# Kernel optimization log

Hardware: AMD Instinct MI355X
Metric: run time of the kernel (lower is better)

Reference implementation:

```python
import jax, jax.numpy as jnp
import numpy as np

SCS = 15000.0          # subcarrier_spacing_hz
FS = 30720000.0        # sampling_freq_hz
FACTOR = 1.5           # ebno_to_snr_factor
MAX_CFO = 0.05
NUM_TAPS = 5
PAD = (NUM_TAPS - 1) // 2

B, N = 64, 131072


def setup_inputs() -> dict:
    key = jax.random.key(0)
    ks = jax.random.split(key, 8)
    return {
        "x_real": jax.random.normal(ks[0], (B, N), jnp.float32),
        "x_imag": jax.random.normal(ks[1], (B, N), jnp.float32),
        "ebno_db": jax.random.uniform(ks[2], (B,), jnp.float32),
        "cfo_u": jax.random.uniform(ks[3], (B, 1), jnp.float32),
        "taps_real": jax.random.normal(ks[4], (B, NUM_TAPS), jnp.float32),
        "taps_imag": jax.random.normal(ks[5], (B, NUM_TAPS), jnp.float32),
        "noise_real": jax.random.normal(ks[6], (B, N), jnp.float32),
        "noise_imag": jax.random.normal(ks[7], (B, N), jnp.float32),
    }


def _depthwise_conv(x, taps):
    # torch F.conv1d (cross-correlation) with groups=batch, padding=PAD.
    # x: [B, N], taps: [B, K] -> y[b, n] = sum_k taps[b, k] * xpad[b, n + k]
    xp = jnp.pad(x, ((0, 0), (PAD, PAD)))
    n = x.shape[1]
    return sum(taps[:, k:k + 1] * xp[:, k:k + n] for k in range(NUM_TAPS))


def _forward(x_real, x_imag, ebno_db, cfo_u, taps_real, taps_imag,
             noise_real, noise_imag):
    # --- Residual CFO: x * exp(i * 2*pi * delta_f * t) ---
    cfo_norm = (cfo_u * 2.0 - 1.0) * MAX_CFO            # [B, 1]
    delta_f = cfo_norm * SCS
    t = jnp.arange(x_real.shape[1], dtype=jnp.float32) / FS  # [N]
    phase = 2.0 * jnp.pi * delta_f * t                  # [B, N]
    c, s = jnp.cos(phase), jnp.sin(phase)
    xr = x_real * c - x_imag * s
    xi = x_real * s + x_imag * c
    # --- TDL fading: complex depthwise conv with per-sample taps ---
    yr = _depthwise_conv(xr, taps_real) - _depthwise_conv(xi, taps_imag)
    yi = _depthwise_conv(xr, taps_imag) + _depthwise_conv(xi, taps_real)
    # --- AWGN ---
    snr_db = ebno_db + 10.0 * jnp.log10(jnp.float32(FACTOR))  # [B]
    noise_std = jnp.sqrt(10.0 ** (-snr_db / 10.0))            # [B]
    # torch.randn_like(complex) has per-component std 1/sqrt(2); scaled by std/sqrt(2)
    scale = (noise_std / 2.0)[:, None]
    yr = yr + noise_real * scale
    yi = yi + noise_imag * scale
    return jnp.stack([yr, yi], axis=0)  # [2, B, N]


def reference(x_real, x_imag, ebno_db, cfo_u, taps_real, taps_imag,
              noise_real, noise_imag):
    return _forward(x_real, x_imag, ebno_db, cfo_u, taps_real, taps_imag,
                    noise_real, noise_imag)
```

## Files before the change

kernel.cpp:

```cpp
#include <hip/hip_runtime.h>
#include <math.h>

#define BB   64
#define NN   131072
#define KTAPS 5
#define TILE 1024
#define NTHREADS 256

#define ANG_PER_HZ 2.0453077171808549e-7f
#define EBNO_OFF   1.7609125905568124f
#define L2TEN_OVER20 0.16609640474436813f

typedef float f32x4 __attribute__((ext_vector_type(4)));

__global__ __launch_bounds__(NTHREADS) void wc_kernel(
    const float* __restrict__ x_real,  const float* __restrict__ x_imag,
    const float* __restrict__ ebno_db, const float* __restrict__ cfo_u,
    const float* __restrict__ taps_real, const float* __restrict__ taps_imag,
    const float* __restrict__ noise_real, const float* __restrict__ noise_imag,
    float* __restrict__ out)
{
    const int b    = blockIdx.y;
    const int base = blockIdx.x * TILE + threadIdx.x * 4;
    const size_t rowoff = (size_t)b * NN;

    const float* __restrict__ xr = x_real + rowoff;
    const float* __restrict__ xi = x_imag + rowoff;

    const int aL = (base == 0)       ? 0        : base - 4;
    const int aR = (base == NN - 4)  ? NN - 4   : base + 4;

    const float4 xrL = *reinterpret_cast<const float4*>(xr + aL);
    const float4 xr0 = *reinterpret_cast<const float4*>(xr + base);
    const float4 xrR = *reinterpret_cast<const float4*>(xr + aR);
    const float4 xiL = *reinterpret_cast<const float4*>(xi + aL);
    const float4 xi0 = *reinterpret_cast<const float4*>(xi + base);
    const float4 xiR = *reinterpret_cast<const float4*>(xi + aR);
    const float4 nr4 = *reinterpret_cast<const float4*>(noise_real + rowoff + base);
    const float4 ni4 = *reinterpret_cast<const float4*>(noise_imag + rowoff + base);

    const float cfo     = cfo_u[b];
    const float delta_f = (cfo * 2.0f - 1.0f) * 0.05f * 15000.0f;
    const float ang     = delta_f * ANG_PER_HZ;
    const float snr     = ebno_db[b] + EBNO_OFF;
    const float scale   = 0.5f * exp2f(-snr * L2TEN_OVER20);

    float tr[KTAPS], ti[KTAPS];
#pragma unroll
    for (int k = 0; k < KTAPS; ++k) {
        tr[k] = taps_real[b * KTAPS + k];
        ti[k] = taps_imag[b * KTAPS + k];
    }

    float sA, cA, s, c;
    sincosf(ang, &sA, &cA);
    sincosf(ang * (float)(base - 2), &s, &c);

    const bool lok = (base != 0);
    const bool rok = (base != NN - 4);

    float ur[8], ui[8];
    ur[0] = lok ? xrL.z : 0.0f;  ui[0] = lok ? xiL.z : 0.0f;
    ur[1] = lok ? xrL.w : 0.0f;  ui[1] = lok ? xiL.w : 0.0f;
    ur[2] = xr0.x;  ui[2] = xi0.x;
    ur[3] = xr0.y;  ui[3] = xi0.y;
    ur[4] = xr0.z;  ui[4] = xi0.z;
    ur[5] = xr0.w;  ui[5] = xi0.w;
    ur[6] = rok ? xrR.x : 0.0f;  ui[6] = rok ? xiR.x : 0.0f;
    ur[7] = rok ? xrR.y : 0.0f;  ui[7] = rok ? xiR.y : 0.0f;

    float wr[8], wi[8];
#pragma unroll
    for (int j = 0; j < 8; ++j) {
        wr[j] = ur[j] * c - ui[j] * s;
        wi[j] = ur[j] * s + ui[j] * c;
        float cn = c * cA - s * sA;
        float sn = s * cA + c * sA;
        c = cn; s = sn;
    }

    const float nr_[4] = {nr4.x, nr4.y, nr4.z, nr4.w};
    const float ni_[4] = {ni4.x, ni4.y, ni4.z, ni4.w};

    f32x4 yr4, yi4;
#pragma unroll
    for (int j = 0; j < 4; ++j) {
        float ar = 0.0f, ai = 0.0f;
#pragma unroll
        for (int k = 0; k < KTAPS; ++k) {
            ar = fmaf(tr[k], wr[j + k], ar);
            ar = fmaf(-ti[k], wi[j + k], ar);
            ai = fmaf(ti[k], wr[j + k], ai);
            ai = fmaf(tr[k], wi[j + k], ai);
        }
        yr4[j] = fmaf(nr_[j], scale, ar);
        yi4[j] = fmaf(ni_[j], scale, ai);
    }

    __builtin_nontemporal_store(yr4, reinterpret_cast<f32x4*>(out + rowoff + base));
    __builtin_nontemporal_store(yi4, reinterpret_cast<f32x4*>(out + (size_t)BB * NN + rowoff + base));
}

extern "C" void kernel_launch(void* const* d_in, const int* in_sizes, int n_in,
                              void* d_out, int out_size, void* d_ws, size_t ws_size,
                              hipStream_t stream) {
    const float* x_real     = (const float*)d_in[0];
    const float* x_imag     = (const float*)d_in[1];
    const float* ebno_db    = (const float*)d_in[2];
    const float* cfo_u      = (const float*)d_in[3];
    const float* taps_real  = (const float*)d_in[4];
    const float* taps_imag  = (const float*)d_in[5];
    const float* noise_real = (const float*)d_in[6];
    const float* noise_imag = (const float*)d_in[7];

    dim3 grid(NN / TILE, BB);
    wc_kernel<<<grid, NTHREADS, 0, stream>>>(
        x_real, x_imag, ebno_db, cfo_u, taps_real, taps_imag,
        noise_real, noise_imag, (float*)d_out);
}
```

Baseline: 180.8 us.

## Process four tiles per block with software-pipelined prefetch and narrower halo loads

Each block now handles four consecutive 1024-element chunks, loading the next chunk's inputs before computing and storing the current one, so loads overlap compute. Halo loads shrink from float4 to float2, which cuts redundant bytes. Per-row setup (taps, sincos of the step angle, noise scale) is amortized over four chunks. The grid shrinks fourfold and register pressure rises, which may reduce occupancy on a purely bandwidth-bound kernel.

```diff
diff --git a/kernel.cpp b/kernel.cpp
--- a/kernel.cpp
+++ b/kernel.cpp
@@ -5,6 +5,8 @@
 #define NN   131072
 #define KTAPS 5
 #define TILE 1024
+#define CHUNKS 4
+#define SPAN (TILE * CHUNKS)
 #define NTHREADS 256
 
 #define ANG_PER_HZ 2.0453077171808549e-7f
@@ -13,61 +15,49 @@
 
 typedef float f32x4 __attribute__((ext_vector_type(4)));
 
-__global__ __launch_bounds__(NTHREADS) void wc_kernel(
-    const float* __restrict__ x_real,  const float* __restrict__ x_imag,
-    const float* __restrict__ ebno_db, const float* __restrict__ cfo_u,
-    const float* __restrict__ taps_real, const float* __restrict__ taps_imag,
-    const float* __restrict__ noise_real, const float* __restrict__ noise_imag,
-    float* __restrict__ out)
-{
-    const int b    = blockIdx.y;
-    const int base = blockIdx.x * TILE + threadIdx.x * 4;
-    const size_t rowoff = (size_t)b * NN;
+struct Buf {
+    float2 xrL, xrR, xiL, xiR;
+    float4 xr0, xi0, nr, ni;
+};
 
-    const float* __restrict__ xr = x_real + rowoff;
-    const float* __restrict__ xi = x_imag + rowoff;
+__device__ __forceinline__ Buf load_chunk(const float* __restrict__ xr,
+                                          const float* __restrict__ xi,
+                                          const float* __restrict__ nr,
+                                          const float* __restrict__ ni,
+                                          int base) {
+    const int aL = (base == 0)      ? 0      : base - 2;
+    const int aR = (base == NN - 4) ? NN - 2 : base + 4;
+    Buf b;
+    b.xrL = *reinterpret_cast<const float2*>(xr + aL);
+    b.xr0 = *reinterpret_cast<const float4*>(xr + base);
+    b.xrR = *reinterpret_cast<const float2*>(xr + aR);
+    b.xiL = *reinterpret_cast<const float2*>(xi + aL);
+    b.xi0 = *reinterpret_cast<const float4*>(xi + base);
+    b.xiR = *reinterpret_cast<const float2*>(xi + aR);
+    b.nr  = *reinterpret_cast<const float4*>(nr + base);
+    b.ni  = *reinterpret_cast<const float4*>(ni + base);
+    return b;
+}
 
-    const int aL = (base == 0)       ? 0        : base - 4;
-    const int aR = (base == NN - 4)  ? NN - 4   : base + 4;
-
-    const float4 xrL = *reinterpret_cast<const float4*>(xr + aL);
-    const float4 xr0 = *reinterpret_cast<const float4*>(xr + base);
-    const float4 xrR = *reinterpret_cast<const float4*>(xr + aR);
-    const float4 xiL = *reinterpret_cast<const float4*>(xi + aL);
-    const float4 xi0 = *reinterpret_cast<const float4*>(xi + base);
-    const float4 xiR = *reinterpret_cast<const float4*>(xi + aR);
-    const float4 nr4 = *reinterpret_cast<const float4*>(noise_real + rowoff + base);
-    const float4 ni4 = *reinterpret_cast<const float4*>(noise_imag + rowoff + base);
-
-    const float cfo     = cfo_u[b];
-    const float delta_f = (cfo * 2.0f - 1.0f) * 0.05f * 15000.0f;
-    const float ang     = delta_f * ANG_PER_HZ;
-    const float snr     = ebno_db[b] + EBNO_OFF;
-    const float scale   = 0.5f * exp2f(-snr * L2TEN_OVER20);
-
-    float tr[KTAPS], ti[KTAPS];
-#pragma unroll
-    for (int k = 0; k < KTAPS; ++k) {
-        tr[k] = taps_real[b * KTAPS + k];
-        ti[k] = taps_imag[b * KTAPS + k];
-    }
-
-    float sA, cA, s, c;
-    sincosf(ang, &sA, &cA);
+__device__ __forceinline__ void compute_store(
+    const Buf& v, int base, float ang, float sA, float cA, float scale,
+    const float* tr, const float* ti, float* __restrict__ outr,
+    float* __restrict__ outi) {
+    float s, c;
     sincosf(ang * (float)(base - 2), &s, &c);
 
     const bool lok = (base != 0);
     const bool rok = (base != NN - 4);
 
     float ur[8], ui[8];
-    ur[0] = lok ? xrL.z : 0.0f;  ui[0] = lok ? xiL.z : 0.0f;
-    ur[1] = lok ? xrL.w : 0.0f;  ui[1] = lok ? xiL.w : 0.0f;
-    ur[2] = xr0.x;  ui[2] = xi0.x;
-    ur[3] = xr0.y;  ui[3] = xi0.y;
-    ur[4] = xr0.z;  ui[4] = xi0.z;
-    ur[5] = xr0.w;  ui[5] = xi0.w;
-    ur[6] = rok ? xrR.x : 0.0f;  ui[6] = rok ? xiR.x : 0.0f;
-    ur[7] = rok ? xrR.y : 0.0f;  ui[7] = rok ? xiR.y : 0.0f;
+    ur[0] = lok ? v.xrL.x : 0.0f;  ui[0] = lok ? v.xiL.x : 0.0f;
+    ur[1] = lok ? v.xrL.y : 0.0f;  ui[1] = lok ? v.xiL.y : 0.0f;
+    ur[2] = v.xr0.x;  ui[2] = v.xi0.x;
+    ur[3] = v.xr0.y;  ui[3] = v.xi0.y;
+    ur[4] = v.xr0.z;  ui[4] = v.xi0.z;
+    ur[5] = v.xr0.w;  ui[5] = v.xi0.w;
+    ur[6] = rok ? v.xrR.x : 0.0f;  ui[6] = rok ? v.xiR.x : 0.0f;
+    ur[7] = rok ? v.xrR.y : 0.0f;  ui[7] = rok ? v.xiR.y : 0.0f;
 
     float wr[8], wi[8];
 #pragma unroll
@@ -79,8 +69,8 @@
         c = cn; s = sn;
     }
 
-    const float nr_[4] = {nr4.x, nr4.y, nr4.z, nr4.w};
-    const float ni_[4] = {ni4.x, ni4.y, ni4.z, ni4.w};
+    const float nr_[4] = {v.nr.x, v.nr.y, v.nr.z, v.nr.w};
+    const float ni_[4] = {v.ni.x, v.ni.y, v.ni.z, v.ni.w};
 
     f32x4 yr4, yi4;
 #pragma unroll
@@ -97,8 +87,54 @@
         yi4[j] = fmaf(ni_[j], scale, ai);
     }
 
-    __builtin_nontemporal_store(yr4, reinterpret_cast<f32x4*>(out + rowoff + base));
-    __builtin_nontemporal_store(yi4, reinterpret_cast<f32x4*>(out + (size_t)BB * NN + rowoff + base));
+    __builtin_nontemporal_store(yr4, reinterpret_cast<f32x4*>(outr + base));
+    __builtin_nontemporal_store(yi4, reinterpret_cast<f32x4*>(outi + base));
+}
+
+__global__ __launch_bounds__(NTHREADS) void wc_kernel(
+    const float* __restrict__ x_real,  const float* __restrict__ x_imag,
+    const float* __restrict__ ebno_db, const float* __restrict__ cfo_u,
+    const float* __restrict__ taps_real, const float* __restrict__ taps_imag,
+    const float* __restrict__ noise_real, const float* __restrict__ noise_imag,
+    float* __restrict__ out)
+{
+    const int b     = blockIdx.y;
+    const int base0 = blockIdx.x * SPAN + threadIdx.x * 4;
+    const size_t rowoff = (size_t)b * NN;
+
+    const float* __restrict__ xr = x_real + rowoff;
+    const float* __restrict__ xi = x_imag + rowoff;
+    const float* __restrict__ nr = noise_real + rowoff;
+    const float* __restrict__ ni = noise_imag + rowoff;
+    float* __restrict__ outr = out + rowoff;
+    float* __restrict__ outi = out + (size_t)BB * NN + rowoff;
+
+    Buf A = load_chunk(xr, xi, nr, ni, base0);
+
+    const float cfo     = cfo_u[b];
+    const float delta_f = (cfo * 2.0f - 1.0f) * 0.05f * 15000.0f;
+    const float ang     = delta_f * ANG_PER_HZ;
+    const float snr     = ebno_db[b] + EBNO_OFF;
+    const float scale   = 0.5f * exp2f(-snr * L2TEN_OVER20);
+
+    float tr[KTAPS], ti[KTAPS];
+#pragma unroll
+    for (int k = 0; k < KTAPS; ++k) {
+        tr[k] = taps_real[b * KTAPS + k];
+        ti[k] = taps_imag[b * KTAPS + k];
+    }
+
+    float sA, cA;
+    sincosf(ang, &sA, &cA);
+
+    Buf B;
+#pragma unroll
+    for (int c = 0; c < CHUNKS; ++c) {
+        if (c + 1 < CHUNKS)
+            B = load_chunk(xr, xi, nr, ni, base0 + (c + 1) * TILE);
+        compute_store(A, base0 + c * TILE, ang, sA, cA, scale, tr, ti, outr, outi);
+        A = B;
+    }
 }
 
 extern "C" void kernel_launch(void* const* d_in, const int* in_sizes, int n_in,
@@ -113,7 +149,7 @@
     const float* noise_real = (const float*)d_in[6];
     const float* noise_imag = (const float*)d_in[7];
 
-    dim3 grid(NN / TILE, BB);
+    dim3 grid(NN / SPAN, BB);
     wc_kernel<<<grid, NTHREADS, 0, stream>>>(
         x_real, x_imag, ebno_db, cfo_u, taps_real, taps_imag,
         noise_real, noise_imag, (float*)d_out);
```

Result: no change. 183.9 us (+1.7%).

## Process multiple tiles per thread with register prefetch and narrower halo loads

Applied to the files above, without the earlier changes.

Each thread now processes four consecutive tiles, prefetching the next tile's signal data into registers while computing the current one, and advances the CFO phasor across tiles with a rotation. Halo loads shrink from float4 to float2, and noise is read with nontemporal loads. The intent is to raise memory-level parallelism and cut redundant loads and per-thread sincos setup. The trade-off is fewer blocks in the grid and higher register pressure, plus a small rounding drift in the phasor recurrence.

```diff
diff --git a/kernel.cpp b/kernel.cpp
--- a/kernel.cpp
+++ b/kernel.cpp
@@ -5,6 +5,8 @@
 #define NN   131072
 #define KTAPS 5
 #define TILE 1024
+#define CHUNKS 4
+#define SPAN (TILE * CHUNKS)
 #define NTHREADS 256
 
 #define ANG_PER_HZ 2.0453077171808549e-7f
@@ -13,7 +15,23 @@
 
 typedef float f32x4 __attribute__((ext_vector_type(4)));
 
-__global__ __launch_bounds__(NTHREADS) void wc_kernel(
+struct XBuf { float4 xr0, xi0; float2 xrL, xrR, xiL, xiR; };
+
+__device__ __forceinline__ XBuf load_x(const float* __restrict__ xr,
+                                       const float* __restrict__ xi, int base) {
+    const int aL = (base == 0)      ? 0      : base - 2;
+    const int aR = (base == NN - 4) ? NN - 2 : base + 4;
+    XBuf v;
+    v.xrL = *reinterpret_cast<const float2*>(xr + aL);
+    v.xr0 = *reinterpret_cast<const float4*>(xr + base);
+    v.xrR = *reinterpret_cast<const float2*>(xr + aR);
+    v.xiL = *reinterpret_cast<const float2*>(xi + aL);
+    v.xi0 = *reinterpret_cast<const float4*>(xi + base);
+    v.xiR = *reinterpret_cast<const float2*>(xi + aR);
+    return v;
+}
+
+__global__ __launch_bounds__(NTHREADS, 8) void wc_kernel(
     const float* __restrict__ x_real,  const float* __restrict__ x_imag,
     const float* __restrict__ ebno_db, const float* __restrict__ cfo_u,
     const float* __restrict__ taps_real, const float* __restrict__ taps_imag,
@@ -21,23 +39,17 @@
     float* __restrict__ out)
 {
     const int b    = blockIdx.y;
-    const int base = blockIdx.x * TILE + threadIdx.x * 4;
+    const int col0 = blockIdx.x * SPAN + threadIdx.x * 4;
     const size_t rowoff = (size_t)b * NN;
 
     const float* __restrict__ xr = x_real + rowoff;
     const float* __restrict__ xi = x_imag + rowoff;
+    const float* __restrict__ nr = noise_real + rowoff;
+    const float* __restrict__ ni = noise_imag + rowoff;
+    float* __restrict__ outr = out + rowoff;
+    float* __restrict__ outi = out + (size_t)BB * NN + rowoff;
 
-    const int aL = (base == 0)       ? 0        : base - 4;
-    const int aR = (base == NN - 4)  ? NN - 4   : base + 4;
-
-    const float4 xrL = *reinterpret_cast<const float4*>(xr + aL);
-    const float4 xr0 = *reinterpret_cast<const float4*>(xr + base);
-    const float4 xrR = *reinterpret_cast<const float4*>(xr + aR);
-    const float4 xiL = *reinterpret_cast<const float4*>(xi + aL);
-    const float4 xi0 = *reinterpret_cast<const float4*>(xi + base);
-    const float4 xiR = *reinterpret_cast<const float4*>(xi + aR);
-    const float4 nr4 = *reinterpret_cast<const float4*>(noise_real + rowoff + base);
-    const float4 ni4 = *reinterpret_cast<const float4*>(noise_imag + rowoff + base);
+    XBuf A = load_x(xr, xi, col0);
 
     const float cfo     = cfo_u[b];
     const float delta_f = (cfo * 2.0f - 1.0f) * 0.05f * 15000.0f;
@@ -52,53 +64,69 @@
         ti[k] = taps_imag[b * KTAPS + k];
     }
 
-    float sA, cA, s, c;
+    float sA, cA, sT, cT, s0, c0;
     sincosf(ang, &sA, &cA);
-    sincosf(ang * (float)(base - 2), &s, &c);
+    sincosf(ang * (float)TILE, &sT, &cT);
+    sincosf(ang * (float)(col0 - 2), &s0, &c0);
 
-    const bool lok = (base != 0);
-    const bool rok = (base != NN - 4);
+    XBuf B = A;
+#pragma unroll
+    for (int ch = 0; ch < CHUNKS; ++ch) {
+        const int base = col0 + ch * TILE;
 
-    float ur[8], ui[8];
-    ur[0] = lok ? xrL.z : 0.0f;  ui[0] = lok ? xiL.z : 0.0f;
-    ur[1] = lok ? xrL.w : 0.0f;  ui[1] = lok ? xiL.w : 0.0f;
-    ur[2] = xr0.x;  ui[2] = xi0.x;
-    ur[3] = xr0.y;  ui[3] = xi0.y;
-    ur[4] = xr0.z;  ui[4] = xi0.z;
-    ur[5] = xr0.w;  ui[5] = xi0.w;
-    ur[6] = rok ? xrR.x : 0.0f;  ui[6] = rok ? xiR.x : 0.0f;
-    ur[7] = rok ? xrR.y : 0.0f;  ui[7] = rok ? xiR.y : 0.0f;
+        if (ch + 1 < CHUNKS) B = load_x(xr, xi, base + TILE);
 
-    float wr[8], wi[8];
+        f32x4 nr4 = __builtin_nontemporal_load(reinterpret_cast<const f32x4*>(nr + base));
+        f32x4 ni4 = __builtin_nontemporal_load(reinterpret_cast<const f32x4*>(ni + base));
+
+        const bool lok = (base != 0);
+        const bool rok = (base != NN - 4);
+
+        float ur[8], ui[8];
+        ur[0] = lok ? A.xrL.x : 0.0f;  ui[0] = lok ? A.xiL.x : 0.0f;
+        ur[1] = lok ? A.xrL.y : 0.0f;  ui[1] = lok ? A.xiL.y : 0.0f;
+        ur[2] = A.xr0.x;  ui[2] = A.xi0.x;
+        ur[3] = A.xr0.y;  ui[3] = A.xi0.y;
+        ur[4] = A.xr0.z;  ui[4] = A.xi0.z;
+        ur[5] = A.xr0.w;  ui[5] = A.xi0.w;
+        ur[6] = rok ? A.xrR.x : 0.0f;  ui[6] = rok ? A.xiR.x : 0.0f;
+        ur[7] = rok ? A.xrR.y : 0.0f;  ui[7] = rok ? A.xiR.y : 0.0f;
+
+        float c = c0, s = s0;
+        float wr[8], wi[8];
 #pragma unroll
-    for (int j = 0; j < 8; ++j) {
-        wr[j] = ur[j] * c - ui[j] * s;
-        wi[j] = ur[j] * s + ui[j] * c;
-        float cn = c * cA - s * sA;
-        float sn = s * cA + c * sA;
-        c = cn; s = sn;
+        for (int j = 0; j < 8; ++j) {
+            wr[j] = ur[j] * c - ui[j] * s;
+            wi[j] = ur[j] * s + ui[j] * c;
+            float cn = c * cA - s * sA;
+            float sn = s * cA + c * sA;
+            c = cn; s = sn;
+        }
+
+        f32x4 yr4, yi4;
+#pragma unroll
+        for (int j = 0; j < 4; ++j) {
+            float ar = 0.0f, ai = 0.0f;
+#pragma unroll
+            for (int k = 0; k < KTAPS; ++k) {
+                ar = fmaf(tr[k], wr[j + k], ar);
+                ar = fmaf(-ti[k], wi[j + k], ar);
+                ai = fmaf(ti[k], wr[j + k], ai);
+                ai = fmaf(tr[k], wi[j + k], ai);
+            }
+            yr4[j] = fmaf(nr4[j], scale, ar);
+            yi4[j] = fmaf(ni4[j], scale, ai);
+        }
+
+        __builtin_nontemporal_store(yr4, reinterpret_cast<f32x4*>(outr + base));
+        __builtin_nontemporal_store(yi4, reinterpret_cast<f32x4*>(outi + base));
+
+        float cn = c0 * cT - s0 * sT;
+        float sn = s0 * cT + c0 * sT;
+        c0 = cn; s0 = sn;
+
+        A = B;
     }
-
-    const float nr_[4] = {nr4.x, nr4.y, nr4.z, nr4.w};
-    const float ni_[4] = {ni4.x, ni4.y, ni4.z, ni4.w};
-
-    f32x4 yr4, yi4;
-#pragma unroll
-    for (int j = 0; j < 4; ++j) {
-        float ar = 0.0f, ai = 0.0f;
-#pragma unroll
-        for (int k = 0; k < KTAPS; ++k) {
-            ar = fmaf(tr[k], wr[j + k], ar);
-            ar = fmaf(-ti[k], wi[j + k], ar);
-            ai = fmaf(ti[k], wr[j + k], ai);
-            ai = fmaf(tr[k], wi[j + k], ai);
-        }
-        yr4[j] = fmaf(nr_[j], scale, ar);
-        yi4[j] = fmaf(ni_[j], scale, ai);
-    }
-
-    __builtin_nontemporal_store(yr4, reinterpret_cast<f32x4*>(out + rowoff + base));
-    __builtin_nontemporal_store(yi4, reinterpret_cast<f32x4*>(out + (size_t)BB * NN + rowoff + base));
 }
 
 extern "C" void kernel_launch(void* const* d_in, const int* in_sizes, int n_in,
@@ -113,7 +141,7 @@
     const float* noise_real = (const float*)d_in[6];
     const float* noise_imag = (const float*)d_in[7];
 
-    dim3 grid(NN / TILE, BB);
+    dim3 grid(NN / SPAN, BB);
     wc_kernel<<<grid, NTHREADS, 0, stream>>>(
         x_real, x_imag, ebno_db, cfo_u, taps_real, taps_imag,
         noise_real, noise_imag, (float*)d_out);
```

Result: slower. 203.0 us (+12.3%).
